# Kernel optimization log

Measured on AMD Instinct MI355X. Metric: run time of the kernel, lower is better.

## Reference

```python
import jax, jax.numpy as jnp
import numpy as np

N = 50000      # nodes
E = 600000     # edges
D = 128        # num_features == hidden_units
L = 4          # num_layers
C = 10         # num_classes
G = 512        # graphs in batch
BN_EPS = 1e-5


def setup_inputs() -> dict:
    key = jax.random.key(0)
    ks = jax.random.split(key, 10)
    x = jax.random.normal(ks[0], (N, D), dtype=jnp.float32)
    src = jax.random.randint(ks[1], (E,), 0, N)
    dst = jax.random.randint(ks[2], (E,), 0, N)
    edge_index = jnp.stack([src, dst]).astype(jnp.int64)
    batch = jnp.sort(jax.random.randint(ks[3], (N,), 0, G)).astype(jnp.int64)
    s = 1.0 / np.sqrt(D)
    Wc1 = jax.random.uniform(ks[4], (L, D, D), jnp.float32, -s, s)
    bc1 = jnp.zeros((L, D), jnp.float32)
    Wc2 = jax.random.uniform(ks[5], (L, D, D), jnp.float32, -s, s)
    bc2 = jnp.zeros((L, D), jnp.float32)
    g_mid = jnp.ones((L, D), jnp.float32)   # BN gamma inside conv MLP
    b_mid = jnp.zeros((L, D), jnp.float32)
    g_out = jnp.ones((L, D), jnp.float32)   # BN gamma after conv
    b_out = jnp.zeros((L, D), jnp.float32)
    fcW = jax.random.uniform(ks[6], (L + 1, D, C), jnp.float32, -s, s)
    fcb = jnp.zeros((L + 1, C), jnp.float32)
    return dict(x=x, edge_index=edge_index, batch=batch, Wc1=Wc1, bc1=bc1,
                Wc2=Wc2, bc2=bc2, g_mid=g_mid, b_mid=b_mid, g_out=g_out,
                b_out=b_out, fcW=fcW, fcb=fcb)


def _bn(h, gamma, beta):
    # training-mode BatchNorm1d over the node axis (biased variance)
    mu = h.mean(0)
    var = h.var(0)
    return (h - mu) * jax.lax.rsqrt(var + BN_EPS) * gamma + beta


def reference(x, edge_index, batch, Wc1, bc1, Wc2, bc2, g_mid, b_mid,
              g_out, b_out, fcW, fcb):
    src, dst = edge_index[0], edge_index[1]
    outs = [x]
    h = x
    for i in range(L):
        # GINConv (eps=0): nn( x + sum_{j in N(i)} x_j )
        agg = jax.ops.segment_sum(h[src], dst, num_segments=N)
        z = h + agg
        z = z @ Wc1[i] + bc1[i]
        z = jax.nn.relu(_bn(z, g_mid[i], b_mid[i]))
        z = z @ Wc2[i] + bc2[i]
        h = jax.nn.relu(_bn(z, g_out[i], b_out[i]))  # outer BN + ReLU
        outs.append(h)
    out = jnp.zeros((G, C), x.dtype)
    for i, o in enumerate(outs):
        pooled = jax.ops.segment_sum(o, batch, num_segments=G)  # [G, D]
        out = out + pooled @ fcW[i] + fcb[i]  # dropout p=0.0 -> identity
    return jax.nn.log_softmax(out, axis=-1)
```

## Files before the change

### kernel.cpp

```cpp
#include <hip/hip_runtime.h>
#include <hip/hip_bf16.h>

#define NN 50000
#define EE 600000
#define DD 128
#define LL 4
#define CC 10
#define GG 512
#define BN_EPS 1e-5f

typedef __attribute__((ext_vector_type(8))) short short8;
typedef __attribute__((ext_vector_type(4))) float f32x4;

__device__ __forceinline__ unsigned short f2b(float f) {
    union { float f; unsigned int u; } v; v.f = f;
    unsigned int u = v.u;
    unsigned int r = (u + 0x7fffu + ((u >> 16) & 1u)) >> 16;
    return (unsigned short)r;
}
__device__ __forceinline__ float b2f(unsigned short h) {
    union { unsigned int u; float f; } v; v.u = ((unsigned int)h) << 16;
    return v.f;
}


__global__ __launch_bounds__(256) void prep_weights(const float* __restrict__ Wc1,
                                                    const float* __restrict__ Wc2,
                                                    unsigned short* __restrict__ WTb) {
    int idx = blockIdx.x * 256 + threadIdx.x;
    int mat = idx >> 14;
    int n = (idx >> 7) & 127;
    int k = idx & 127;
    const float* srcp = (mat < 4) ? (Wc1 + (size_t)mat * DD * DD)
                                  : (Wc2 + (size_t)(mat - 4) * DD * DD);
    WTb[idx] = f2b(srcp[k * DD + n]);
}


__global__ void hist_kernel(const int* __restrict__ idx, int* __restrict__ cnt, int n) {
    int i = blockIdx.x * blockDim.x + threadIdx.x;
    if (i < n) atomicAdd(&cnt[idx[i]], 1);
}

__global__ __launch_bounds__(256) void block_sums(const int* __restrict__ in,
                                                  int* __restrict__ bsums, int n) {
    __shared__ int red[256];
    int b = blockIdx.x, t = threadIdx.x;
    int base = b * 1024 + t * 4;
    int s = 0;
    if (base + 3 < n) {
        int4 v = *(const int4*)(in + base);
        s = v.x + v.y + v.z + v.w;
    } else {
        for (int i = 0; i < 4; ++i) if (base + i < n) s += in[base + i];
    }
    red[t] = s;
    __syncthreads();
    for (int off = 128; off > 0; off >>= 1) {
        if (t < off) red[t] += red[t + off];
        __syncthreads();
    }
    if (t == 0) bsums[b] = red[0];
}

__global__ __launch_bounds__(256) void scan_bsums(int* __restrict__ bsums, int nb) {
    __shared__ int red[256];
    int t = threadIdx.x;
    int v = (t < nb) ? bsums[t] : 0;
    red[t] = v;
    __syncthreads();
    for (int off = 1; off < 256; off <<= 1) {
        int u = (t >= off) ? red[t - off] : 0;
        __syncthreads();
        red[t] += u;
        __syncthreads();
    }
    if (t < nb) bsums[t] = red[t] - v;
    if (t == 0) bsums[nb] = red[255];
}

__global__ __launch_bounds__(256) void scan_final(const int* __restrict__ in,
                                                  const int* __restrict__ bsums,
                                                  int* __restrict__ out,
                                                  int* __restrict__ out2, int n) {
    __shared__ int red[256];
    int b = blockIdx.x, t = threadIdx.x;
    int base = b * 1024 + t * 4;
    int v[4];
    int s = 0;
#pragma unroll
    for (int i = 0; i < 4; ++i) {
        v[i] = (base + i < n) ? in[base + i] : 0;
        s += v[i];
    }
    red[t] = s;
    __syncthreads();
    for (int off = 1; off < 256; off <<= 1) {
        int u = (t >= off) ? red[t - off] : 0;
        __syncthreads();
        red[t] += u;
        __syncthreads();
    }
    int run = bsums[b] + red[t] - s;
#pragma unroll
    for (int i = 0; i < 4; ++i) {
        if (base + i < n) {
            out[base + i] = run;
            if (out2) out2[base + i] = run;
            run += v[i];
        }
    }
    if (b == (int)gridDim.x - 1 && t == 255) out[n] = run;
}

__global__ void fill_csr(const int* __restrict__ src, const int* __restrict__ dst,
                         int* __restrict__ cursor, int* __restrict__ csr) {
    int e = blockIdx.x * blockDim.x + threadIdx.x;
    if (e < EE) {
        int d = dst[e];
        int pos = atomicAdd(&cursor[d], 1);
        csr[pos] = src[e];
    }
}

__global__ void gptr_search(const int* __restrict__ batch, int* __restrict__ gptr) {
    int g = blockIdx.x * blockDim.x + threadIdx.x;
    if (g > GG) return;
    int lo = 0, hi = NN;
    while (lo < hi) {
        int mid = (lo + hi) >> 1;
        if (batch[mid] < g) lo = mid + 1; else hi = mid;
    }
    gptr[g] = lo;
}


template <bool BN>
__global__ __launch_bounds__(256) void aggregate_k(const unsigned short* __restrict__ hb,
                                                   const int* __restrict__ rowptr,
                                                   const int* __restrict__ csr,
                                                   const float* __restrict__ stats,
                                                   const float* __restrict__ gamma,
                                                   const float* __restrict__ beta,
                                                   unsigned short* __restrict__ outb) {
    int node = blockIdx.x * 4 + (threadIdx.x >> 6);
    if (node >= NN) return;
    const int lane = threadIdx.x & 63;
    const int seg = lane & 15;
    const int slot = lane >> 4;

    float A[8], B[8];
    if (BN) {
#pragma unroll
        for (int j = 0; j < 8; ++j) {
            int c = seg * 8 + j;
            float mu = stats[c] * (1.0f / NN);
            float var = stats[DD + c] * (1.0f / NN) - mu * mu;
            A[j] = gamma[c] * rsqrtf(var + BN_EPS);
            B[j] = beta[c] - mu * A[j];
        }
    }

    const uint4* hb4 = (const uint4*)hb;
    uint4 self = hb4[(size_t)node * 16 + seg];

    float acc[8];
#pragma unroll
    for (int j = 0; j < 8; ++j) acc[j] = 0.f;

    const int beg = rowptr[node], end = rowptr[node + 1];
    for (int e = beg; e < end; e += 16) {
        int idx[4];
        bool val[4];
#pragma unroll
        for (int i = 0; i < 4; ++i) {
            int t = e + i * 4 + slot;
            val[i] = (t < end);
            idx[i] = csr[val[i] ? t : beg];
        }
        uint4 v[4];
#pragma unroll
        for (int i = 0; i < 4; ++i) v[i] = hb4[(size_t)idx[i] * 16 + seg];
#pragma unroll
        for (int i = 0; i < 4; ++i) {
            if (val[i]) {
#pragma unroll
                for (int j = 0; j < 4; ++j) {
                    unsigned int u = ((unsigned int*)&v[i])[j];
                    float x = b2f((unsigned short)(u & 0xffff));
                    float y = b2f((unsigned short)(u >> 16));
                    if (BN) {
                        x = fmaxf(0.f, fmaf(x, A[2 * j], B[2 * j]));
                        y = fmaxf(0.f, fmaf(y, A[2 * j + 1], B[2 * j + 1]));
                    }
                    acc[2 * j] += x;
                    acc[2 * j + 1] += y;
                }
            }
        }
    }

#pragma unroll
    for (int j = 0; j < 8; ++j) {
        acc[j] += __shfl_xor(acc[j], 16);
        acc[j] += __shfl_xor(acc[j], 32);
    }

    if (slot == 0) {
        uint4 o;
#pragma unroll
        for (int j = 0; j < 4; ++j) {
            unsigned int u = ((unsigned int*)&self)[j];
            float x = b2f((unsigned short)(u & 0xffff));
            float y = b2f((unsigned short)(u >> 16));
            if (BN) {
                x = fmaxf(0.f, fmaf(x, A[2 * j], B[2 * j]));
                y = fmaxf(0.f, fmaf(y, A[2 * j + 1], B[2 * j + 1]));
            }
            ((unsigned int*)&o)[j] =
                (unsigned int)f2b(acc[2 * j] + x) | ((unsigned int)f2b(acc[2 * j + 1] + y) << 16);
        }
        ((uint4*)outb)[(size_t)node * 16 + seg] = o;
    }
}


__global__ __launch_bounds__(256) void gemm_mfma(
    const unsigned short* __restrict__ Ab,
    const unsigned short* __restrict__ WTb,
    const float* __restrict__ bias,
    const float* __restrict__ bnStatsIn,
    const float* __restrict__ gamma, const float* __restrict__ beta,
    unsigned short* __restrict__ Outb,
    float* __restrict__ statsOut)
{
    __shared__ unsigned short As[128 * 128];
    __shared__ unsigned short Bs[128 * 128];
    __shared__ float AbnS[DD], BbnS[DD];
    __shared__ float colred[2][DD];

    const int tid = threadIdx.x;
    const int row0 = blockIdx.x * 128;
    const bool doBn = (bnStatsIn != nullptr);

    if (tid < DD) {
        colred[0][tid] = 0.f;
        colred[1][tid] = 0.f;
        if (doBn) {
            float mu = bnStatsIn[tid] * (1.0f / NN);
            float var = bnStatsIn[DD + tid] * (1.0f / NN) - mu * mu;
            float A = gamma[tid] * rsqrtf(var + BN_EPS);
            AbnS[tid] = A;
            BbnS[tid] = beta[tid] - mu * A;
        }
    }
    __syncthreads();

    const uint4* Bg = (const uint4*)WTb;
#pragma unroll
    for (int i = 0; i < 8; ++i) {
        int c = tid + i * 256;
        int row = c >> 4, seg = c & 15;
        uint4 v = Bg[c];
        int byte = (row * 256 + seg * 16) ^ ((row & 7) << 4);
        *(uint4*)((char*)Bs + byte) = v;
    }
#pragma unroll
    for (int i = 0; i < 8; ++i) {
        int c = tid + i * 256;
        int row = c >> 4, seg = c & 15;
        int gr = row0 + row;
        uint4 v = make_uint4(0u, 0u, 0u, 0u);
        if (gr < NN) v = ((const uint4*)(Ab + (size_t)gr * DD))[seg];
        if (doBn) {
            int k0 = seg * 8;
#pragma unroll
            for (int e = 0; e < 4; ++e) {
                unsigned int u = ((unsigned int*)&v)[e];
                int cidx = k0 + 2 * e;
                float lo = fmaxf(0.f, fmaf(b2f((unsigned short)(u & 0xffff)), AbnS[cidx], BbnS[cidx]));
                float hi = fmaxf(0.f, fmaf(b2f((unsigned short)(u >> 16)), AbnS[cidx + 1], BbnS[cidx + 1]));
                ((unsigned int*)&v)[e] = (unsigned int)f2b(lo) | ((unsigned int)f2b(hi) << 16);
            }
        }
        int byte = (row * 256 + seg * 16) ^ ((row & 7) << 4);
        *(uint4*)((char*)As + byte) = v;
    }
    __syncthreads();

    const int wave = tid >> 6, lane = tid & 63;
    const int fr = lane & 15, fq = lane >> 4;
    const int wr0 = wave * 32;

    f32x4 acc[2][8];
#pragma unroll
    for (int m = 0; m < 2; ++m)
#pragma unroll
        for (int n = 0; n < 8; ++n) acc[m][n] = (f32x4)0.f;

#pragma unroll
    for (int kk = 0; kk < 4; ++kk) {
        int kbyte = kk * 64 + fq * 16;
        short8 a[2], b[8];
#pragma unroll
        for (int m = 0; m < 2; ++m) {
            int row = wr0 + m * 16 + fr;
            a[m] = *(const short8*)((const char*)As + ((row * 256 + kbyte) ^ ((row & 7) << 4)));
        }
#pragma unroll
        for (int n = 0; n < 8; ++n) {
            int row = n * 16 + fr;
            b[n] = *(const short8*)((const char*)Bs + ((row * 256 + kbyte) ^ ((row & 7) << 4)));
        }
#pragma unroll
        for (int m = 0; m < 2; ++m)
#pragma unroll
            for (int n = 0; n < 8; ++n)
                acc[m][n] = __builtin_amdgcn_mfma_f32_16x16x32_bf16(a[m], b[n], acc[m][n], 0, 0, 0);
    }

    float bias_n[8], s[8], q[8];
#pragma unroll
    for (int n = 0; n < 8; ++n) {
        bias_n[n] = bias[n * 16 + fr];
        s[n] = 0.f;
        q[n] = 0.f;
    }
#pragma unroll
    for (int m = 0; m < 2; ++m) {
        int rbase = row0 + wr0 + m * 16 + fq * 4;
#pragma unroll
        for (int j = 0; j < 4; ++j) {
            int gr = rbase + j;
            if (gr < NN) {
#pragma unroll
                for (int n = 0; n < 8; ++n) {
                    float o = acc[m][n][j] + bias_n[n];
                    Outb[(size_t)gr * DD + n * 16 + fr] = f2b(o);
                    s[n] += o;
                    q[n] += o * o;
                }
            }
        }
    }
    if (statsOut) {
#pragma unroll
        for (int n = 0; n < 8; ++n) {
            s[n] += __shfl_xor(s[n], 16);
            s[n] += __shfl_xor(s[n], 32);
            q[n] += __shfl_xor(q[n], 16);
            q[n] += __shfl_xor(q[n], 32);
        }
        if (fq == 0) {
#pragma unroll
            for (int n = 0; n < 8; ++n) {
                atomicAdd(&colred[0][n * 16 + fr], s[n]);
                atomicAdd(&colred[1][n * 16 + fr], q[n]);
            }
        }
        __syncthreads();
        if (tid < DD) {
            atomicAdd(&statsOut[tid], colred[0][tid]);
            atomicAdd(&statsOut[DD + tid], colred[1][tid]);
        }
    }
}


__global__ __launch_bounds__(256) void bn_pool(const unsigned short* __restrict__ Z,
                                               const float* __restrict__ stats,
                                               const float* __restrict__ gamma,
                                               const float* __restrict__ beta,
                                               const int* __restrict__ gptr,
                                               float* __restrict__ pooledDst) {
    __shared__ float2 red[4][64];
    int g = blockIdx.x;
    int wave = threadIdx.x >> 6, lane = threadIdx.x & 63;
    int c0 = lane * 2, c1 = c0 + 1;
    float mu0 = stats[c0] * (1.0f / NN);
    float var0 = stats[DD + c0] * (1.0f / NN) - mu0 * mu0;
    float A0 = gamma[c0] * rsqrtf(var0 + BN_EPS);
    float B0 = beta[c0] - mu0 * A0;
    float mu1 = stats[c1] * (1.0f / NN);
    float var1 = stats[DD + c1] * (1.0f / NN) - mu1 * mu1;
    float A1 = gamma[c1] * rsqrtf(var1 + BN_EPS);
    float B1 = beta[c1] - mu1 * A1;

    float ax = 0.f, ay = 0.f;
    int beg = gptr[g], end = gptr[g + 1];
    for (int r = beg + wave; r < end; r += 4) {
        unsigned int u = ((const unsigned int*)(Z + (size_t)r * DD))[lane];
        ax += fmaxf(0.f, fmaf(b2f((unsigned short)(u & 0xffff)), A0, B0));
        ay += fmaxf(0.f, fmaf(b2f((unsigned short)(u >> 16)), A1, B1));
    }
    red[wave][lane] = make_float2(ax, ay);
    __syncthreads();
    if (threadIdx.x < 64) {
        float2 a = red[0][lane], b = red[1][lane], c = red[2][lane], d = red[3][lane];
        ((float2*)pooledDst)[(size_t)g * 64 + lane] =
            make_float2(a.x + b.x + c.x + d.x, a.y + b.y + c.y + d.y);
    }
}


__global__ __launch_bounds__(256) void cvt_pool_x(const float* __restrict__ x,
                                                  const int* __restrict__ gptr,
                                                  unsigned short* __restrict__ xb,
                                                  float* __restrict__ dst) {
    __shared__ float2 red[4][64];
    int g = blockIdx.x;
    int wave = threadIdx.x >> 6, lane = threadIdx.x & 63;
    float ax = 0.f, ay = 0.f;
    int beg = gptr[g], end = gptr[g + 1];
    for (int r = beg + wave; r < end; r += 4) {
        float2 v = ((const float2*)(x + (size_t)r * DD))[lane];
        ax += v.x; ay += v.y;
        ((unsigned int*)(xb + (size_t)r * DD))[lane] =
            (unsigned int)f2b(v.x) | ((unsigned int)f2b(v.y) << 16);
    }
    red[wave][lane] = make_float2(ax, ay);
    __syncthreads();
    if (threadIdx.x < 64) {
        float2 a = red[0][lane], b = red[1][lane], c = red[2][lane], d = red[3][lane];
        ((float2*)dst)[(size_t)g * 64 + lane] =
            make_float2(a.x + b.x + c.x + d.x, a.y + b.y + c.y + d.y);
    }
}


__global__ __launch_bounds__(64) void final_kernel(const float* __restrict__ pooled,
                                                   const float* __restrict__ fcW,
                                                   const float* __restrict__ fcb,
                                                   float* __restrict__ out) {
    int g = blockIdx.x;
    int lane = threadIdx.x;
    float acc[CC];
#pragma unroll
    for (int c = 0; c < CC; ++c) acc[c] = 0.f;
    for (int i = 0; i < LL + 1; ++i) {
        const float* P = pooled + ((size_t)i * GG + g) * DD;
        const float* Wf = fcW + (size_t)i * DD * CC;
        for (int k = lane; k < DD; k += 64) {
            float p = P[k];
            const float* wr = Wf + k * CC;
#pragma unroll
            for (int c = 0; c < CC; ++c) acc[c] = fmaf(p, wr[c], acc[c]);
        }
    }
#pragma unroll
    for (int c = 0; c < CC; ++c)
        for (int off = 32; off > 0; off >>= 1) acc[c] += __shfl_down(acc[c], off);
    if (lane == 0) {
#pragma unroll
        for (int c = 0; c < CC; ++c) {
            float b = 0.f;
            for (int i = 0; i < LL + 1; ++i) b += fcb[i * CC + c];
            acc[c] += b;
        }
        float m = acc[0];
#pragma unroll
        for (int c = 1; c < CC; ++c) m = fmaxf(m, acc[c]);
        float se = 0.f;
#pragma unroll
        for (int c = 0; c < CC; ++c) se += expf(acc[c] - m);
        float lse = m + logf(se);
#pragma unroll
        for (int c = 0; c < CC; ++c) out[(size_t)g * CC + c] = acc[c] - lse;
    }
}


extern "C" void kernel_launch(void* const* d_in, const int* in_sizes, int n_in,
                              void* d_out, int out_size, void* d_ws, size_t ws_size,
                              hipStream_t stream) {
    const float* x     = (const float*)d_in[0];
    const int*   ei    = (const int*)d_in[1];
    const int*   batch = (const int*)d_in[2];
    const float* Wc1   = (const float*)d_in[3];
    const float* bc1   = (const float*)d_in[4];
    const float* Wc2   = (const float*)d_in[5];
    const float* bc2   = (const float*)d_in[6];
    const float* g_mid = (const float*)d_in[7];
    const float* b_mid = (const float*)d_in[8];
    const float* g_out = (const float*)d_in[9];
    const float* b_out = (const float*)d_in[10];
    const float* fcW   = (const float*)d_in[11];
    const float* fcb   = (const float*)d_in[12];
    float* out = (float*)d_out;

    char* p = (char*)d_ws;
    unsigned short* xb   = (unsigned short*)p; p += (size_t)NN * DD * 2;
    unsigned short* aggb = (unsigned short*)p; p += (size_t)NN * DD * 2;
    unsigned short* z1b  = (unsigned short*)p; p += (size_t)NN * DD * 2;
    unsigned short* z2b  = (unsigned short*)p; p += (size_t)NN * DD * 2;
    unsigned short* WTb  = (unsigned short*)p; p += (size_t)8 * DD * DD * 2;
    float* pooled = (float*)p; p += (size_t)(LL + 1) * GG * DD * 4;
    float* statb  = (float*)p; p += 8 * 256 * 4;
    int* deg    = (int*)p; p += (size_t)NN * 4;
    int* rowptr = (int*)p; p += (size_t)(NN + 16) * 4;
    int* cursor = (int*)p; p += (size_t)NN * 4;
    int* csr    = (int*)p; p += (size_t)EE * 4;
    int* gptr   = (int*)p; p += (size_t)(GG + 16) * 4;
    int* bsum1  = (int*)p; p += 64 * 4;

    hipMemsetAsync(statb, 0, (size_t)(8 * 256) * 4 + (size_t)NN * 4, stream);

    const int* src = ei;
    const int* dst = ei + EE;

    prep_weights<<<(8 * DD * DD) / 256, 256, 0, stream>>>(Wc1, Wc2, WTb);

    hist_kernel<<<(EE + 255) / 256, 256, 0, stream>>>(dst, deg, EE);
    const int nb = (NN + 1023) / 1024;
    block_sums<<<nb, 256, 0, stream>>>(deg, bsum1, NN);
    scan_bsums<<<1, 256, 0, stream>>>(bsum1, nb);
    scan_final<<<nb, 256, 0, stream>>>(deg, bsum1, rowptr, cursor, NN);
    fill_csr<<<(EE + 255) / 256, 256, 0, stream>>>(src, dst, cursor, csr);
    gptr_search<<<3, 256, 0, stream>>>(batch, gptr);
    cvt_pool_x<<<GG, 256, 0, stream>>>(x, gptr, xb, pooled);

    const int gemmGrid = (NN + 127) / 128;
    const int aggGrid = (NN + 3) / 4;
    for (int l = 0; l < LL; ++l) {
        if (l == 0) {
            aggregate_k<false><<<aggGrid, 256, 0, stream>>>(
                xb, rowptr, csr, nullptr, nullptr, nullptr, aggb);
        } else {
            aggregate_k<true><<<aggGrid, 256, 0, stream>>>(
                z2b, rowptr, csr, statb + (size_t)(2 * (l - 1) + 1) * 256,
                g_out + (size_t)(l - 1) * DD, b_out + (size_t)(l - 1) * DD, aggb);
        }
        gemm_mfma<<<gemmGrid, 256, 0, stream>>>(
            aggb, WTb + (size_t)l * DD * DD, bc1 + (size_t)l * DD,
            nullptr, nullptr, nullptr,
            z1b, statb + (size_t)(2 * l) * 256);
        gemm_mfma<<<gemmGrid, 256, 0, stream>>>(
            z1b, WTb + (size_t)(4 + l) * DD * DD, bc2 + (size_t)l * DD,
            statb + (size_t)(2 * l) * 256, g_mid + (size_t)l * DD, b_mid + (size_t)l * DD,
            z2b, statb + (size_t)(2 * l + 1) * 256);
        bn_pool<<<GG, 256, 0, stream>>>(
            z2b, statb + (size_t)(2 * l + 1) * 256,
            g_out + (size_t)l * DD, b_out + (size_t)l * DD, gptr,
            pooled + (size_t)(l + 1) * GG * DD);
    }
    final_kernel<<<GG, 64, 0, stream>>>(pooled, fcW, fcb, out);
}
```

Before: 418.9 us.

## Fuse setup and post-layer kernels, hold GEMM weight fragments in registers

Merges the histogram, weight-prep and graph-pointer search into one launch. Merges BN+pool with the next layer's aggregation, and the last pooling with the final classifier, into block-partitioned kernels. The GEMM now loads its B fragments straight from global memory into registers instead of staging them in shared memory, which halves LDS use, and sets launch bounds for two blocks per SM. This cuts launch count and LDS traffic, at the cost of higher register pressure in the GEMM.

```diff
diff --git a/kernel.cpp b/kernel.cpp
--- a/kernel.cpp
+++ b/kernel.cpp
@@ -9,6 +9,10 @@
 #define GG 512
 #define BN_EPS 1e-5f
 
+#define HB_BLOCKS ((EE + 255) / 256)
+#define PW_BLOCKS ((8 * DD * DD) / 256)
+#define AGG_BLOCKS ((NN + 3) / 4)
+
 typedef __attribute__((ext_vector_type(8))) short short8;
 typedef __attribute__((ext_vector_type(4))) float f32x4;
 
@@ -24,23 +28,37 @@
 }
 
 
-__global__ __launch_bounds__(256) void prep_weights(const float* __restrict__ Wc1,
+__global__ __launch_bounds__(256) void setup_kernel(const int* __restrict__ dst,
+                                                    int* __restrict__ deg,
+                                                    const float* __restrict__ Wc1,
                                                     const float* __restrict__ Wc2,
-                                                    unsigned short* __restrict__ WTb) {
-    int idx = blockIdx.x * 256 + threadIdx.x;
-    int mat = idx >> 14;
-    int n = (idx >> 7) & 127;
-    int k = idx & 127;
-    const float* srcp = (mat < 4) ? (Wc1 + (size_t)mat * DD * DD)
-                                  : (Wc2 + (size_t)(mat - 4) * DD * DD);
-    WTb[idx] = f2b(srcp[k * DD + n]);
-}
-
-
-__global__ void hist_kernel(const int* __restrict__ idx, int* __restrict__ cnt, int n) {
-    int i = blockIdx.x * blockDim.x + threadIdx.x;
-    if (i < n) atomicAdd(&cnt[idx[i]], 1);
-}
+                                                    unsigned short* __restrict__ WTb,
+                                                    const int* __restrict__ batch,
+                                                    int* __restrict__ gptr) {
+    int b = blockIdx.x;
+    if (b < HB_BLOCKS) {
+        int i = b * 256 + threadIdx.x;
+        if (i < EE) atomicAdd(&deg[dst[i]], 1);
+    } else if (b < HB_BLOCKS + PW_BLOCKS) {
+        int idx = (b - HB_BLOCKS) * 256 + threadIdx.x;
+        int mat = idx >> 14;
+        int n = (idx >> 7) & 127;
+        int k = idx & 127;
+        const float* srcp = (mat < 4) ? (Wc1 + (size_t)mat * DD * DD)
+                                      : (Wc2 + (size_t)(mat - 4) * DD * DD);
+        WTb[idx] = f2b(srcp[k * DD + n]);
+    } else {
+        int g = (b - HB_BLOCKS - PW_BLOCKS) * 256 + threadIdx.x;
+        if (g > GG) return;
+        int lo = 0, hi = NN;
+        while (lo < hi) {
+            int mid = (lo + hi) >> 1;
+            if (batch[mid] < g) lo = mid + 1; else hi = mid;
+        }
+        gptr[g] = lo;
+    }
+}
+
 
 __global__ __launch_bounds__(256) void block_sums(const int* __restrict__ in,
                                                   int* __restrict__ bsums, int n) {
@@ -123,28 +141,15 @@
     }
 }
 
-__global__ void gptr_search(const int* __restrict__ batch, int* __restrict__ gptr) {
-    int g = blockIdx.x * blockDim.x + threadIdx.x;
-    if (g > GG) return;
-    int lo = 0, hi = NN;
-    while (lo < hi) {
-        int mid = (lo + hi) >> 1;
-        if (batch[mid] < g) lo = mid + 1; else hi = mid;
-    }
-    gptr[g] = lo;
-}
-
 
 template <bool BN>
-__global__ __launch_bounds__(256) void aggregate_k(const unsigned short* __restrict__ hb,
-                                                   const int* __restrict__ rowptr,
-                                                   const int* __restrict__ csr,
-                                                   const float* __restrict__ stats,
-                                                   const float* __restrict__ gamma,
-                                                   const float* __restrict__ beta,
-                                                   unsigned short* __restrict__ outb) {
-    int node = blockIdx.x * 4 + (threadIdx.x >> 6);
-    if (node >= NN) return;
+__device__ __forceinline__ void agg_node(int node, const unsigned short* __restrict__ hb,
+                                         const int* __restrict__ rowptr,
+                                         const int* __restrict__ csr,
+                                         const float* __restrict__ stats,
+                                         const float* __restrict__ gamma,
+                                         const float* __restrict__ beta,
+                                         unsigned short* __restrict__ outb) {
     const int lane = threadIdx.x & 63;
     const int seg = lane & 15;
     const int slot = lane >> 4;
@@ -224,8 +229,17 @@
     }
 }
 
-
-__global__ __launch_bounds__(256) void gemm_mfma(
+__global__ __launch_bounds__(256) void aggregate_x(const unsigned short* __restrict__ hb,
+                                                   const int* __restrict__ rowptr,
+                                                   const int* __restrict__ csr,
+                                                   unsigned short* __restrict__ outb) {
+    int node = blockIdx.x * 4 + (threadIdx.x >> 6);
+    if (node >= NN) return;
+    agg_node<false>(node, hb, rowptr, csr, nullptr, nullptr, nullptr, outb);
+}
+
+
+__global__ __launch_bounds__(256, 2) void gemm_mfma(
     const unsigned short* __restrict__ Ab,
     const unsigned short* __restrict__ WTb,
     const float* __restrict__ bias,
@@ -235,13 +249,21 @@
     float* __restrict__ statsOut)
 {
     __shared__ unsigned short As[128 * 128];
-    __shared__ unsigned short Bs[128 * 128];
     __shared__ float AbnS[DD], BbnS[DD];
     __shared__ float colred[2][DD];
 
     const int tid = threadIdx.x;
     const int row0 = blockIdx.x * 128;
     const bool doBn = (bnStatsIn != nullptr);
+    const int lane = tid & 63;
+    const int fr = lane & 15, fq = lane >> 4;
+
+    short8 bfrag[8][4];
+#pragma unroll
+    for (int n = 0; n < 8; ++n)
+#pragma unroll
+        for (int kk = 0; kk < 4; ++kk)
+            bfrag[n][kk] = *(const short8*)((const char*)WTb + (n * 16 + fr) * 256 + kk * 64 + fq * 16);
 
     if (tid < DD) {
         colred[0][tid] = 0.f;
@@ -254,17 +276,8 @@
             BbnS[tid] = beta[tid] - mu * A;
         }
     }
-    __syncthreads();
-
-    const uint4* Bg = (const uint4*)WTb;
-#pragma unroll
-    for (int i = 0; i < 8; ++i) {
-        int c = tid + i * 256;
-        int row = c >> 4, seg = c & 15;
-        uint4 v = Bg[c];
-        int byte = (row * 256 + seg * 16) ^ ((row & 7) << 4);
-        *(uint4*)((char*)Bs + byte) = v;
-    }
+    if (doBn) __syncthreads();
+
 #pragma unroll
     for (int i = 0; i < 8; ++i) {
         int c = tid + i * 256;
@@ -288,8 +301,7 @@
     }
     __syncthreads();
 
-    const int wave = tid >> 6, lane = tid & 63;
-    const int fr = lane & 15, fq = lane >> 4;
+    const int wave = tid >> 6;
     const int wr0 = wave * 32;
 
     f32x4 acc[2][8];
@@ -301,22 +313,17 @@
 #pragma unroll
     for (int kk = 0; kk < 4; ++kk) {
         int kbyte = kk * 64 + fq * 16;
-        short8 a[2], b[8];
+        short8 a[2];
 #pragma unroll
         for (int m = 0; m < 2; ++m) {
             int row = wr0 + m * 16 + fr;
             a[m] = *(const short8*)((const char*)As + ((row * 256 + kbyte) ^ ((row & 7) << 4)));
         }
 #pragma unroll
-        for (int n = 0; n < 8; ++n) {
-            int row = n * 16 + fr;
-            b[n] = *(const short8*)((const char*)Bs + ((row * 256 + kbyte) ^ ((row & 7) << 4)));
-        }
-#pragma unroll
         for (int m = 0; m < 2; ++m)
 #pragma unroll
             for (int n = 0; n < 8; ++n)
-                acc[m][n] = __builtin_amdgcn_mfma_f32_16x16x32_bf16(a[m], b[n], acc[m][n], 0, 0, 0);
+                acc[m][n] = __builtin_amdgcn_mfma_f32_16x16x32_bf16(a[m], bfrag[n][kk], acc[m][n], 0, 0, 0);
     }
 
     float bias_n[8], s[8], q[8];
@@ -343,62 +350,119 @@
             }
         }
     }
-    if (statsOut) {
+#pragma unroll
+    for (int n = 0; n < 8; ++n) {
+        s[n] += __shfl_xor(s[n], 16);
+        s[n] += __shfl_xor(s[n], 32);
+        q[n] += __shfl_xor(q[n], 16);
+        q[n] += __shfl_xor(q[n], 32);
+    }
+    if (fq == 0) {
 #pragma unroll
         for (int n = 0; n < 8; ++n) {
-            s[n] += __shfl_xor(s[n], 16);
-            s[n] += __shfl_xor(s[n], 32);
-            q[n] += __shfl_xor(q[n], 16);
-            q[n] += __shfl_xor(q[n], 32);
-        }
-        if (fq == 0) {
-#pragma unroll
-            for (int n = 0; n < 8; ++n) {
-                atomicAdd(&colred[0][n * 16 + fr], s[n]);
-                atomicAdd(&colred[1][n * 16 + fr], q[n]);
+            atomicAdd(&colred[0][n * 16 + fr], s[n]);
+            atomicAdd(&colred[1][n * 16 + fr], q[n]);
+        }
+    }
+    __syncthreads();
+    if (tid < DD) {
+        atomicAdd(&statsOut[tid], colred[0][tid]);
+        atomicAdd(&statsOut[DD + tid], colred[1][tid]);
+    }
+}
+
+
+template <bool LAST>
+__global__ __launch_bounds__(256) void post_layer(
+    const unsigned short* __restrict__ Z,
+    const float* __restrict__ stats,
+    const float* __restrict__ gamma,
+    const float* __restrict__ beta,
+    const int* __restrict__ gptr,
+    const int* __restrict__ rowptr,
+    const int* __restrict__ csr,
+    float* __restrict__ pooledDst,
+    unsigned short* __restrict__ aggOut,
+    const float* __restrict__ pooledAll,
+    const float* __restrict__ fcW,
+    const float* __restrict__ fcb,
+    float* __restrict__ out)
+{
+    const int bid = blockIdx.x;
+    if (bid < GG) {
+        __shared__ float2 red[4][64];
+        __shared__ float p4[DD];
+        const int g = bid;
+        const int wave = threadIdx.x >> 6, lane = threadIdx.x & 63;
+        const int c0 = lane * 2, c1 = c0 + 1;
+        float mu0 = stats[c0] * (1.0f / NN);
+        float var0 = stats[DD + c0] * (1.0f / NN) - mu0 * mu0;
+        float A0 = gamma[c0] * rsqrtf(var0 + BN_EPS);
+        float B0 = beta[c0] - mu0 * A0;
+        float mu1 = stats[c1] * (1.0f / NN);
+        float var1 = stats[DD + c1] * (1.0f / NN) - mu1 * mu1;
+        float A1 = gamma[c1] * rsqrtf(var1 + BN_EPS);
+        float B1 = beta[c1] - mu1 * A1;
+
+        float ax = 0.f, ay = 0.f;
+        int beg = gptr[g], end = gptr[g + 1];
+        for (int r = beg + wave; r < end; r += 4) {
+            unsigned int u = ((const unsigned int*)(Z + (size_t)r * DD))[lane];
+            ax += fmaxf(0.f, fmaf(b2f((unsigned short)(u & 0xffff)), A0, B0));
+            ay += fmaxf(0.f, fmaf(b2f((unsigned short)(u >> 16)), A1, B1));
+        }
+        red[wave][lane] = make_float2(ax, ay);
+        __syncthreads();
+        if (threadIdx.x < 64) {
+            float2 a = red[0][lane], b = red[1][lane], c = red[2][lane], d = red[3][lane];
+            float2 r2 = make_float2(a.x + b.x + c.x + d.x, a.y + b.y + c.y + d.y);
+            ((float2*)pooledDst)[(size_t)g * 64 + lane] = r2;
+            if (LAST) {
+                p4[c0] = r2.x;
+                p4[c1] = r2.y;
             }
         }
-        __syncthreads();
-        if (tid < DD) {
-            atomicAdd(&statsOut[tid], colred[0][tid]);
-            atomicAdd(&statsOut[DD + tid], colred[1][tid]);
-        }
-    }
-}
-
-
-__global__ __launch_bounds__(256) void bn_pool(const unsigned short* __restrict__ Z,
-                                               const float* __restrict__ stats,
-                                               const float* __restrict__ gamma,
-                                               const float* __restrict__ beta,
-                                               const int* __restrict__ gptr,
-                                               float* __restrict__ pooledDst) {
-    __shared__ float2 red[4][64];
-    int g = blockIdx.x;
-    int wave = threadIdx.x >> 6, lane = threadIdx.x & 63;
-    int c0 = lane * 2, c1 = c0 + 1;
-    float mu0 = stats[c0] * (1.0f / NN);
-    float var0 = stats[DD + c0] * (1.0f / NN) - mu0 * mu0;
-    float A0 = gamma[c0] * rsqrtf(var0 + BN_EPS);
-    float B0 = beta[c0] - mu0 * A0;
-    float mu1 = stats[c1] * (1.0f / NN);
-    float var1 = stats[DD + c1] * (1.0f / NN) - mu1 * mu1;
-    float A1 = gamma[c1] * rsqrtf(var1 + BN_EPS);
-    float B1 = beta[c1] - mu1 * A1;
-
-    float ax = 0.f, ay = 0.f;
-    int beg = gptr[g], end = gptr[g + 1];
-    for (int r = beg + wave; r < end; r += 4) {
-        unsigned int u = ((const unsigned int*)(Z + (size_t)r * DD))[lane];
-        ax += fmaxf(0.f, fmaf(b2f((unsigned short)(u & 0xffff)), A0, B0));
-        ay += fmaxf(0.f, fmaf(b2f((unsigned short)(u >> 16)), A1, B1));
-    }
-    red[wave][lane] = make_float2(ax, ay);
-    __syncthreads();
-    if (threadIdx.x < 64) {
-        float2 a = red[0][lane], b = red[1][lane], c = red[2][lane], d = red[3][lane];
-        ((float2*)pooledDst)[(size_t)g * 64 + lane] =
-            make_float2(a.x + b.x + c.x + d.x, a.y + b.y + c.y + d.y);
+        if (LAST) {
+            __syncthreads();
+            if (threadIdx.x < 64) {
+                float acc[CC];
+#pragma unroll
+                for (int c = 0; c < CC; ++c) acc[c] = 0.f;
+                for (int i = 0; i < LL + 1; ++i) {
+                    const float* Wf = fcW + (size_t)i * DD * CC;
+                    for (int k = lane; k < DD; k += 64) {
+                        float pv = (i == LL) ? p4[k] : pooledAll[((size_t)i * GG + g) * DD + k];
+                        const float* wr = Wf + k * CC;
+#pragma unroll
+                        for (int c = 0; c < CC; ++c) acc[c] = fmaf(pv, wr[c], acc[c]);
+                    }
+                }
+#pragma unroll
+                for (int c = 0; c < CC; ++c)
+                    for (int off = 32; off > 0; off >>= 1) acc[c] += __shfl_down(acc[c], off);
+                if (lane == 0) {
+#pragma unroll
+                    for (int c = 0; c < CC; ++c) {
+                        float b = 0.f;
+                        for (int i = 0; i < LL + 1; ++i) b += fcb[i * CC + c];
+                        acc[c] += b;
+                    }
+                    float m = acc[0];
+#pragma unroll
+                    for (int c = 1; c < CC; ++c) m = fmaxf(m, acc[c]);
+                    float se = 0.f;
+#pragma unroll
+                    for (int c = 0; c < CC; ++c) se += expf(acc[c] - m);
+                    float lse = m + logf(se);
+#pragma unroll
+                    for (int c = 0; c < CC; ++c) out[(size_t)g * CC + c] = acc[c] - lse;
+                }
+            }
+        }
+    } else {
+        int node = (bid - GG) * 4 + (threadIdx.x >> 6);
+        if (node >= NN) return;
+        agg_node<true>(node, Z, rowptr, csr, stats, gamma, beta, aggOut);
     }
 }
 
@@ -424,48 +488,6 @@
         float2 a = red[0][lane], b = red[1][lane], c = red[2][lane], d = red[3][lane];
         ((float2*)dst)[(size_t)g * 64 + lane] =
             make_float2(a.x + b.x + c.x + d.x, a.y + b.y + c.y + d.y);
-    }
-}
-
-
-__global__ __launch_bounds__(64) void final_kernel(const float* __restrict__ pooled,
-                                                   const float* __restrict__ fcW,
-                                                   const float* __restrict__ fcb,
-                                                   float* __restrict__ out) {
-    int g = blockIdx.x;
-    int lane = threadIdx.x;
-    float acc[CC];
-#pragma unroll
-    for (int c = 0; c < CC; ++c) acc[c] = 0.f;
-    for (int i = 0; i < LL + 1; ++i) {
-        const float* P = pooled + ((size_t)i * GG + g) * DD;
-        const float* Wf = fcW + (size_t)i * DD * CC;
-        for (int k = lane; k < DD; k += 64) {
-            float p = P[k];
-            const float* wr = Wf + k * CC;
-#pragma unroll
-            for (int c = 0; c < CC; ++c) acc[c] = fmaf(p, wr[c], acc[c]);
-        }
-    }
-#pragma unroll
-    for (int c = 0; c < CC; ++c)
-        for (int off = 32; off > 0; off >>= 1) acc[c] += __shfl_down(acc[c], off);
-    if (lane == 0) {
-#pragma unroll
-        for (int c = 0; c < CC; ++c) {
-            float b = 0.f;
-            for (int i = 0; i < LL + 1; ++i) b += fcb[i * CC + c];
-            acc[c] += b;
-        }
-        float m = acc[0];
-#pragma unroll
-        for (int c = 1; c < CC; ++c) m = fmaxf(m, acc[c]);
-        float se = 0.f;
-#pragma unroll
-        for (int c = 0; c < CC; ++c) se += expf(acc[c] - m);
-        float lse = m + logf(se);
-#pragma unroll
-        for (int c = 0; c < CC; ++c) out[(size_t)g * CC + c] = acc[c] - lse;
     }
 }
 
@@ -508,28 +530,19 @@
     const int* src = ei;
     const int* dst = ei + EE;
 
-    prep_weights<<<(8 * DD * DD) / 256, 256, 0, stream>>>(Wc1, Wc2, WTb);
-
-    hist_kernel<<<(EE + 255) / 256, 256, 0, stream>>>(dst, deg, EE);
+    setup_kernel<<<HB_BLOCKS + PW_BLOCKS + 3, 256, 0, stream>>>(
+        dst, deg, Wc1, Wc2, WTb, batch, gptr);
+
     const int nb = (NN + 1023) / 1024;
     block_sums<<<nb, 256, 0, stream>>>(deg, bsum1, NN);
     scan_bsums<<<1, 256, 0, stream>>>(bsum1, nb);
     scan_final<<<nb, 256, 0, stream>>>(deg, bsum1, rowptr, cursor, NN);
     fill_csr<<<(EE + 255) / 256, 256, 0, stream>>>(src, dst, cursor, csr);
-    gptr_search<<<3, 256, 0, stream>>>(batch, gptr);
     cvt_pool_x<<<GG, 256, 0, stream>>>(x, gptr, xb, pooled);
 
     const int gemmGrid = (NN + 127) / 128;
-    const int aggGrid = (NN + 3) / 4;
+    aggregate_x<<<AGG_BLOCKS, 256, 0, stream>>>(xb, rowptr, csr, aggb);
     for (int l = 0; l < LL; ++l) {
-        if (l == 0) {
-            aggregate_k<false><<<aggGrid, 256, 0, stream>>>(
-                xb, rowptr, csr, nullptr, nullptr, nullptr, aggb);
-        } else {
-            aggregate_k<true><<<aggGrid, 256, 0, stream>>>(
-                z2b, rowptr, csr, statb + (size_t)(2 * (l - 1) + 1) * 256,
-                g_out + (size_t)(l - 1) * DD, b_out + (size_t)(l - 1) * DD, aggb);
-        }
         gemm_mfma<<<gemmGrid, 256, 0, stream>>>(
             aggb, WTb + (size_t)l * DD * DD, bc1 + (size_t)l * DD,
             nullptr, nullptr, nullptr,
@@ -538,10 +551,20 @@
             z1b, WTb + (size_t)(4 + l) * DD * DD, bc2 + (size_t)l * DD,
             statb + (size_t)(2 * l) * 256, g_mid + (size_t)l * DD, b_mid + (size_t)l * DD,
             z2b, statb + (size_t)(2 * l + 1) * 256);
-        bn_pool<<<GG, 256, 0, stream>>>(
-            z2b, statb + (size_t)(2 * l + 1) * 256,
-            g_out + (size_t)l * DD, b_out + (size_t)l * DD, gptr,
-            pooled + (size_t)(l + 1) * GG * DD);
-    }
-    final_kernel<<<GG, 64, 0, stream>>>(pooled, fcW, fcb, out);
-}
+        if (l < LL - 1) {
+            post_layer<false><<<GG + AGG_BLOCKS, 256, 0, stream>>>(
+                z2b, statb + (size_t)(2 * l + 1) * 256,
+                g_out + (size_t)l * DD, b_out + (size_t)l * DD,
+                gptr, rowptr, csr,
+                pooled + (size_t)(l + 1) * GG * DD, aggb,
+                nullptr, nullptr, nullptr, nullptr);
+        } else {
+            post_layer<true><<<GG, 256, 0, stream>>>(
+                z2b, statb + (size_t)(2 * l + 1) * 256,
+                g_out + (size_t)l * DD, b_out + (size_t)l * DD,
+                gptr, rowptr, csr,
+                pooled + (size_t)(l + 1) * GG * DD, nullptr,
+                pooled, fcW, fcb, out);
+        }
+    }
+}
```

Result: faster. 406.2 us (-3.0%).
